# Performance work log

Hardware: AMD Instinct MI355X
Metric: run time of the kernel (lower is better)

Reference implementation:

```python
import jax, jax.numpy as jnp
import numpy as np

B, S, D = 2, 2048, 1024
E, H = 8, 2816  # hidden = 256*ceil(int(2*(4*1024)/3)/256) = 2816
TOP_K = 2


def setup_inputs() -> dict:
    key = jax.random.key(0)
    k0, k1, k2, k3, k4 = jax.random.split(key, 5)
    x = jax.random.normal(k0, (B, S, D), dtype=jnp.float32)
    wg = jax.random.normal(k1, (D, E), dtype=jnp.float32) * (D ** -0.5)
    w1 = jax.random.normal(k2, (E, D, H), dtype=jnp.float32) * 0.02  # gate proj
    w3 = jax.random.normal(k3, (E, D, H), dtype=jnp.float32) * 0.02  # up proj
    w2 = jax.random.normal(k4, (E, H, D), dtype=jnp.float32) * 0.02  # down proj
    return {"x": x, "wg": wg, "w1": w1, "w2": w2, "w3": w3}


def reference(x, wg, w1, w2, w3):
    Bb, Ss, Dd = x.shape
    Ee = w1.shape[0]
    xf = x.reshape(-1, Dd)                       # [T, D]
    logits = xf @ wg                              # [T, E]
    probs = jax.nn.softmax(logits, axis=-1)
    topk_p, topk_i = jax.lax.top_k(probs, TOP_K)  # [T, K]
    topk_p = topk_p / jnp.sum(topk_p, axis=-1, keepdims=True)
    # combine weight per (token, expert): sum over top-k slots
    cw = jnp.sum(jax.nn.one_hot(topk_i, Ee, dtype=xf.dtype) * topk_p[..., None], axis=1)  # [T, E]
    out = jnp.zeros_like(xf)
    for e in range(Ee):  # fixed small loop over experts
        h = jax.nn.silu(xf @ w1[e]) * (xf @ w3[e])   # [T, H] SwiGLU
        out = out + cw[:, e:e + 1] * (h @ w2[e])     # weighted combine
    return out.reshape(Bb, Ss, Dd)
```

## Files before the change

### kernel.cpp

```cpp
#include <hip/hip_runtime.h>
#include <hip/hip_bf16.h>

typedef unsigned short u16;
typedef __bf16 bf16_t;
typedef bf16_t bf16x8 __attribute__((ext_vector_type(8)));
typedef float f32x4 __attribute__((ext_vector_type(4)));

#define T_TOK 4096
#define DIM   1024
#define NEXP  8
#define HID   2816
#define CAP   16

static __device__ __forceinline__ u16 f2b(float f) {
    __hip_bfloat16 h = __float2bfloat16(f);
    return *(u16*)&h;
}

static __device__ __forceinline__ void glds16(const u16* g, u16* l) {
    __builtin_amdgcn_global_load_lds((const __attribute__((address_space(1))) void*)g,
                                     (__attribute__((address_space(3))) void*)l, 16, 0, 0);
}

__global__ void k_gating(const float* __restrict__ X,
                         const float* __restrict__ WG,
                         int* __restrict__ cnt,
                         int* __restrict__ tok,
                         float* __restrict__ wt,
                         u16* __restrict__ Xbf)
{
    int wv   = threadIdx.x >> 6;
    int lane = threadIdx.x & 63;
    int t = blockIdx.x * 4 + wv;
    float l[NEXP];
#pragma unroll
    for (int e = 0; e < NEXP; ++e) l[e] = 0.f;
#pragma unroll
    for (int i = 0; i < DIM/64; ++i) {
        int d = i*64 + lane;
        float xv = X[(size_t)t*DIM + d];
        Xbf[(size_t)t*DIM + d] = f2b(xv);
        const float* wrow = WG + (size_t)d*NEXP;
        float4 wa = *(const float4*)wrow;
        float4 wb = *(const float4*)(wrow + 4);
        l[0] += xv*wa.x; l[1] += xv*wa.y; l[2] += xv*wa.z; l[3] += xv*wa.w;
        l[4] += xv*wb.x; l[5] += xv*wb.y; l[6] += xv*wb.z; l[7] += xv*wb.w;
    }
#pragma unroll
    for (int e = 0; e < NEXP; ++e) {
#pragma unroll
        for (int s = 32; s > 0; s >>= 1)
            l[e] += __shfl_xor(l[e], s, 64);
    }
    if (lane == 0) {
        int i1 = 0; float b1 = l[0];
#pragma unroll
        for (int e = 1; e < NEXP; ++e) if (l[e] > b1) { b1 = l[e]; i1 = e; }
        int i2 = -1; float b2 = 0.f;
#pragma unroll
        for (int e = 0; e < NEXP; ++e) {
            if (e == i1) continue;
            if (i2 < 0 || l[e] > b2) { b2 = l[e]; i2 = e; }
        }
        float p1 = 1.f / (1.f + __expf(b2 - b1));
        float p2 = 1.f - p1;
        int pos = atomicAdd(&cnt[i1], 1);
        tok[i1*T_TOK + pos] = t;  wt[i1*T_TOK + pos] = p1;
        pos = atomicAdd(&cnt[i2], 1);
        tok[i2*T_TOK + pos] = t;  wt[i2*T_TOK + pos] = p2;
    }
}

__global__ void k_compact(const int* __restrict__ cnt,
                          const int* __restrict__ tok, const float* __restrict__ wt,
                          int* __restrict__ ctok, float* __restrict__ cwt)
{
    int e = blockIdx.x;
    int off = 0;
    for (int i = 0; i < e; ++i) off += cnt[i];
    int n = cnt[e];
    for (int i = threadIdx.x; i < n; i += blockDim.x) {
        ctok[off + i] = tok[e*T_TOK + i];
        cwt [off + i] = wt [e*T_TOK + i];
    }
}

#define TS 72
__global__ void k_transpose_cast(const float* __restrict__ in, u16* __restrict__ out,
                                 int R, int C)
{
    __shared__ u16 tle[64*TS];
    size_t mb = (size_t)blockIdx.z * (size_t)R * C;
    int r0 = blockIdx.x * 64, c0 = blockIdx.y * 64;
    int tid = threadIdx.x;
    const float* I = in + mb + (size_t)r0*C + c0;
#pragma unroll
    for (int p = 0; p < 4; ++p) {
        int q = tid + p*256;
        int r = q >> 4, cc = (q & 15) * 4;
        float4 v = *(const float4*)&I[(size_t)r*C + cc];
        tle[(cc+0)*TS + r] = f2b(v.x);
        tle[(cc+1)*TS + r] = f2b(v.y);
        tle[(cc+2)*TS + r] = f2b(v.z);
        tle[(cc+3)*TS + r] = f2b(v.w);
    }
    __syncthreads();
    u16* O = out + mb + (size_t)c0*R + r0;
    int rc = tid & 7, oc = tid >> 3;
#pragma unroll
    for (int p = 0; p < 2; ++p) {
        int c = oc + p*32;
        *(uint4*)&O[(size_t)c*R + rc*8] = *(const uint4*)&tle[c*TS + rc*8];
    }
}

__global__ __launch_bounds__(256, 3) void k_gemm1(
    const u16* __restrict__ X, const u16* __restrict__ W1t, const u16* __restrict__ W3t,
    u16* __restrict__ Hbuf, const int* __restrict__ cnt, const int* __restrict__ ctok)
{
    __shared__ u16 As[128*32];
    __shared__ u16 Bs[128*32];
    __shared__ int tokLds[128];

    const int bid = blockIdx.x;
    const int e   = bid & 7;
    const int q   = bid >> 3;
    const int mt0 = q & (CAP-1);
    const int col = q >> 4;
    const int ne  = cnt[e];
    const int ntile = (ne + 127) >> 7;
    if (mt0 >= ntile) return;
    int off = 0;
    for (int i = 0; i < e; ++i) off += cnt[i];
    const int h0 = col * 64;

    const int tid = threadIdx.x, wave = tid >> 6, lane = tid & 63;
    const int wr = wave >> 1, wc = wave & 1;
    const int quad = lane >> 4, lr = lane & 15;
    const int lrow = lane >> 2, lko = (lane & 3) * 8;

    const size_t wb = (size_t)e * HID * DIM;
    const u16* w1g = W1t + wb + (size_t)(h0 + wave*16 + lrow)*DIM + lko;
    const u16* w3g = W3t + wb + (size_t)(h0 + wave*16 + lrow)*DIM + lko;
    u16* aL0 = &As[(wave*16)*32];
    u16* aL1 = &As[(64 + wave*16)*32];
    u16* bL0 = &Bs[(wave*16)*32];
    u16* bL1 = &Bs[(64 + wave*16)*32];

    for (int tile = mt0; tile < ntile; tile += CAP) {
        const int m0 = tile << 7;
        int nvalid = ne - m0; if (nvalid > 128) nvalid = 128;

        __syncthreads();
        if (tid < 128) {
            int i = (tid < nvalid) ? tid : (nvalid - 1);
            tokLds[tid] = ctok[off + m0 + i];
        }
        __syncthreads();
        const u16* ag0 = X + (size_t)tokLds[wave*16 + lrow]*DIM + lko;
        const u16* ag1 = X + (size_t)tokLds[64 + wave*16 + lrow]*DIM + lko;

        f32x4 a1[4][2], a3[4][2];
#pragma unroll
        for (int m = 0; m < 4; ++m)
#pragma unroll
            for (int n = 0; n < 2; ++n) {
                a1[m][n] = (f32x4){0.f,0.f,0.f,0.f};
                a3[m][n] = (f32x4){0.f,0.f,0.f,0.f};
            }

        for (int k0 = 0; k0 < DIM; k0 += 32) {
            __syncthreads();
            glds16(ag0 + k0, aL0);
            glds16(ag1 + k0, aL1);
            glds16(w1g + k0, bL0);
            glds16(w3g + k0, bL1);
            __syncthreads();
            bf16x8 af[4], b1[2], b3[2];
#pragma unroll
            for (int m = 0; m < 4; ++m)
                af[m] = *(const bf16x8*)&As[(wr*64 + m*16 + lr)*32 + quad*8];
#pragma unroll
            for (int n = 0; n < 2; ++n) {
                b1[n] = *(const bf16x8*)&Bs[(wc*32 + n*16 + lr)*32 + quad*8];
                b3[n] = *(const bf16x8*)&Bs[(64 + wc*32 + n*16 + lr)*32 + quad*8];
            }
#pragma unroll
            for (int m = 0; m < 4; ++m)
#pragma unroll
                for (int n = 0; n < 2; ++n) {
                    a1[m][n] = __builtin_amdgcn_mfma_f32_16x16x32_bf16(af[m], b1[n], a1[m][n], 0, 0, 0);
                    a3[m][n] = __builtin_amdgcn_mfma_f32_16x16x32_bf16(af[m], b3[n], a3[m][n], 0, 0, 0);
                }
        }

#pragma unroll
        for (int m = 0; m < 4; ++m) {
            int mb_ = wr*64 + m*16 + quad*4;
#pragma unroll
            for (int rr = 0; rr < 4; ++rr) {
                int mm = mb_ + rr;
                if (mm >= nvalid) continue;
                u16* hrow = Hbuf + (size_t)(off + m0 + mm)*HID + h0 + wc*32 + lr;
#pragma unroll
                for (int n = 0; n < 2; ++n) {
                    float g = a1[m][n][rr];
                    float u = a3[m][n][rr];
                    hrow[n*16] = f2b((g / (1.f + __expf(-g))) * u);
                }
            }
        }
    }
}

__global__ __launch_bounds__(256, 3) void k_gemm2(
    const u16* __restrict__ Hbuf, const u16* __restrict__ W2t,
    float* __restrict__ outf, const int* __restrict__ cnt,
    const int* __restrict__ ctok, const float* __restrict__ cwt)
{
    __shared__ u16 As[128*32];
    __shared__ u16 Bs[128*32];
    __shared__ int   tLds[128];
    __shared__ float wLds[128];

    const int bid = blockIdx.x;
    const int e   = bid & 7;
    const int q   = bid >> 3;
    const int mt0 = q & (CAP-1);
    const int r2  = q >> 4;
    const int zk  = r2 & 1;
    const int d0  = (r2 >> 1) * 128;
    const int ne  = cnt[e];
    const int ntile = (ne + 127) >> 7;
    if (mt0 >= ntile) return;
    int off = 0;
    for (int i = 0; i < e; ++i) off += cnt[i];
    const int kb = zk * (HID/2);

    const int tid = threadIdx.x, wave = tid >> 6, lane = tid & 63;
    const int wr = wave >> 1, wc = wave & 1;
    const int quad = lane >> 4, lr = lane & 15;
    const int lrow = lane >> 2, lko = (lane & 3) * 8;

    const size_t w2b = (size_t)e * DIM * HID;
    const u16* bg0 = W2t + w2b + (size_t)(d0 + wave*16 + lrow)*HID + kb + lko;
    const u16* bg1 = bg0 + (size_t)64*HID;
    u16* aL0 = &As[(wave*16)*32];
    u16* aL1 = &As[(64 + wave*16)*32];
    u16* bL0 = &Bs[(wave*16)*32];
    u16* bL1 = &Bs[(64 + wave*16)*32];

    for (int tile = mt0; tile < ntile; tile += CAP) {
        const int m0 = tile << 7;
        int nvalid = ne - m0; if (nvalid > 128) nvalid = 128;

        __syncthreads();
        if (tid < 128) {
            int i = (tid < nvalid) ? tid : (nvalid - 1);
            tLds[tid] = ctok[off + m0 + i];
            wLds[tid] = cwt [off + m0 + i];
        }
        __syncthreads();
        int ar0 = wave*16 + lrow;      if (ar0 >= nvalid) ar0 = nvalid - 1;
        int ar1 = 64 + wave*16 + lrow; if (ar1 >= nvalid) ar1 = nvalid - 1;
        const u16* ag0 = Hbuf + (size_t)(off + m0 + ar0)*HID + kb + lko;
        const u16* ag1 = Hbuf + (size_t)(off + m0 + ar1)*HID + kb + lko;

        f32x4 acc[4][4];
#pragma unroll
        for (int a = 0; a < 4; ++a)
#pragma unroll
            for (int b = 0; b < 4; ++b) acc[a][b] = (f32x4){0.f,0.f,0.f,0.f};

        for (int k0 = 0; k0 < HID/2; k0 += 32) {
            __syncthreads();
            glds16(ag0 + k0, aL0);
            glds16(ag1 + k0, aL1);
            glds16(bg0 + k0, bL0);
            glds16(bg1 + k0, bL1);
            __syncthreads();
            bf16x8 af[4], bf[4];
#pragma unroll
            for (int m = 0; m < 4; ++m)
                af[m] = *(const bf16x8*)&As[(wr*64 + m*16 + lr)*32 + quad*8];
#pragma unroll
            for (int n = 0; n < 4; ++n)
                bf[n] = *(const bf16x8*)&Bs[(wc*64 + n*16 + lr)*32 + quad*8];
#pragma unroll
            for (int m = 0; m < 4; ++m)
#pragma unroll
                for (int n = 0; n < 4; ++n)
                    acc[m][n] = __builtin_amdgcn_mfma_f32_16x16x32_bf16(af[m], bf[n], acc[m][n], 0, 0, 0);
        }

#pragma unroll
        for (int m = 0; m < 4; ++m) {
            int mb_ = wr*64 + m*16 + quad*4;
#pragma unroll
            for (int rr = 0; rr < 4; ++rr) {
                int mm = mb_ + rr;
                if (mm >= nvalid) continue;
                float wr_ = wLds[mm];
                float* orow = outf + (size_t)tLds[mm]*DIM + d0 + wc*64 + lr;
#pragma unroll
                for (int n = 0; n < 4; ++n)
                    atomicAdd(&orow[n*16], acc[m][n][rr] * wr_);
            }
        }
    }
}

extern "C" void kernel_launch(void* const* d_in, const int* in_sizes, int n_in,
                              void* d_out, int out_size, void* d_ws, size_t ws_size,
                              hipStream_t stream)
{
    const float* x  = (const float*)d_in[0];
    const float* wg = (const float*)d_in[1];
    const float* w1 = (const float*)d_in[2];
    const float* w2 = (const float*)d_in[3];
    const float* w3 = (const float*)d_in[4];
    float* outf = (float*)d_out;

    char* ws = (char*)d_ws;
    int*   cnt  = (int*)  (ws);
    int*   tok  = (int*)  (ws + 256);
    float* wt   = (float*)(ws + 131328);
    int*   ctok = (int*)  (ws + 262400);
    float* cwt  = (float*)(ws + 295168);
    u16*   Xbf  = (u16*)  (ws + 327936);
    u16*   Hbuf = (u16*)  (ws + 8716544);
    u16*   W1t  = (u16*)  (ws + 54853888);
    u16*   W3t  = (u16*)  (ws + 100991232);
    u16*   W2t  = (u16*)  (ws + 147128576);

    hipMemsetAsync(cnt, 0, 256, stream);
    hipMemsetAsync(outf, 0, (size_t)T_TOK*DIM*sizeof(float), stream);

    k_transpose_cast<<<dim3(DIM/64, HID/64, NEXP), 256, 0, stream>>>(w1, W1t, DIM, HID);
    k_transpose_cast<<<dim3(DIM/64, HID/64, NEXP), 256, 0, stream>>>(w3, W3t, DIM, HID);
    k_transpose_cast<<<dim3(HID/64, DIM/64, NEXP), 256, 0, stream>>>(w2, W2t, HID, DIM);

    k_gating<<<T_TOK/4, 256, 0, stream>>>(x, wg, cnt, tok, wt, Xbf);
    k_compact<<<NEXP, 256, 0, stream>>>(cnt, tok, wt, ctok, cwt);

    k_gemm1<<<NEXP*(HID/64)*CAP, 256, 0, stream>>>(Xbf, W1t, W3t, Hbuf, cnt, ctok);
    k_gemm2<<<NEXP*CAP*2*(DIM/128), 256, 0, stream>>>(Hbuf, W2t, outf, cnt, ctok, cwt);
}
```

Before: 670.0 us.

## Double GEMM K-tile to 64 with XOR-swizzled LDS and fewer M-tile blocks

Both expert GEMM kernels now stage 64-wide K slices in LDS instead of 32, which halves the number of barrier pairs per tile. Each lane now issues four 16-byte direct-to-LDS loads per operand. The 16-byte chunks are XOR-swizzled by row so the MFMA fragment reads avoid LDS bank conflicts. The M-tile cap per expert drops from 16 to 8, so fewer blocks are launched and each loops over more tiles. The trade-off is double the LDS per block, which could limit occupancy, and worse load balance for experts that receive many tokens.

```diff
diff --git a/kernel.cpp b/kernel.cpp
--- a/kernel.cpp
+++ b/kernel.cpp
@@ -10,7 +10,8 @@
 #define DIM   1024
 #define NEXP  8
 #define HID   2816
-#define CAP   16
+#define CAP   8
+#define CAPL  3
 
 static __device__ __forceinline__ u16 f2b(float f) {
     __hip_bfloat16 h = __float2bfloat16(f);
@@ -118,15 +119,15 @@
     const u16* __restrict__ X, const u16* __restrict__ W1t, const u16* __restrict__ W3t,
     u16* __restrict__ Hbuf, const int* __restrict__ cnt, const int* __restrict__ ctok)
 {
-    __shared__ u16 As[128*32];
-    __shared__ u16 Bs[128*32];
+    __shared__ u16 As[128*64];
+    __shared__ u16 Bs[128*64];
     __shared__ int tokLds[128];
 
     const int bid = blockIdx.x;
     const int e   = bid & 7;
     const int q   = bid >> 3;
     const int mt0 = q & (CAP-1);
-    const int col = q >> 4;
+    const int col = q >> CAPL;
     const int ne  = cnt[e];
     const int ntile = (ne + 127) >> 7;
     if (mt0 >= ntile) return;
@@ -137,15 +138,15 @@
     const int tid = threadIdx.x, wave = tid >> 6, lane = tid & 63;
     const int wr = wave >> 1, wc = wave & 1;
     const int quad = lane >> 4, lr = lane & 15;
-    const int lrow = lane >> 2, lko = (lane & 3) * 8;
+    const int lrow8 = lane >> 3;
+    const int sw = ((lane & 7) ^ lrow8) * 8;
 
     const size_t wb = (size_t)e * HID * DIM;
-    const u16* w1g = W1t + wb + (size_t)(h0 + wave*16 + lrow)*DIM + lko;
-    const u16* w3g = W3t + wb + (size_t)(h0 + wave*16 + lrow)*DIM + lko;
-    u16* aL0 = &As[(wave*16)*32];
-    u16* aL1 = &As[(64 + wave*16)*32];
-    u16* bL0 = &Bs[(wave*16)*32];
-    u16* bL1 = &Bs[(64 + wave*16)*32];
+    const u16* Wsel = (wave < 2) ? W1t : W3t;
+    const u16* bp[4];
+#pragma unroll
+    for (int c = 0; c < 4; ++c)
+        bp[c] = Wsel + wb + (size_t)(h0 + (wave & 1)*32 + c*8 + lrow8)*DIM + sw;
 
     for (int tile = mt0; tile < ntile; tile += CAP) {
         const int m0 = tile << 7;
@@ -157,8 +158,10 @@
             tokLds[tid] = ctok[off + m0 + i];
         }
         __syncthreads();
-        const u16* ag0 = X + (size_t)tokLds[wave*16 + lrow]*DIM + lko;
-        const u16* ag1 = X + (size_t)tokLds[64 + wave*16 + lrow]*DIM + lko;
+        const u16* ap[4];
+#pragma unroll
+        for (int c = 0; c < 4; ++c)
+            ap[c] = X + (size_t)tokLds[wave*32 + c*8 + lrow8]*DIM + sw;
 
         f32x4 a1[4][2], a3[4][2];
 #pragma unroll
@@ -169,29 +172,34 @@
                 a3[m][n] = (f32x4){0.f,0.f,0.f,0.f};
             }
 
-        for (int k0 = 0; k0 < DIM; k0 += 32) {
+        for (int k0 = 0; k0 < DIM; k0 += 64) {
             __syncthreads();
-            glds16(ag0 + k0, aL0);
-            glds16(ag1 + k0, aL1);
-            glds16(w1g + k0, bL0);
-            glds16(w3g + k0, bL1);
+#pragma unroll
+            for (int c = 0; c < 4; ++c) {
+                glds16(ap[c] + k0, &As[(wave*32 + c*8)*64]);
+                glds16(bp[c] + k0, &Bs[(wave*32 + c*8)*64]);
+            }
             __syncthreads();
-            bf16x8 af[4], b1[2], b3[2];
-#pragma unroll
-            for (int m = 0; m < 4; ++m)
-                af[m] = *(const bf16x8*)&As[(wr*64 + m*16 + lr)*32 + quad*8];
-#pragma unroll
-            for (int n = 0; n < 2; ++n) {
-                b1[n] = *(const bf16x8*)&Bs[(wc*32 + n*16 + lr)*32 + quad*8];
-                b3[n] = *(const bf16x8*)&Bs[(64 + wc*32 + n*16 + lr)*32 + quad*8];
-            }
-#pragma unroll
-            for (int m = 0; m < 4; ++m)
+#pragma unroll
+            for (int kk = 0; kk < 2; ++kk) {
+                const int jx = ((kk*4 + quad) ^ (lr & 7)) * 8;
+                bf16x8 af[4], b1[2], b3[2];
+#pragma unroll
+                for (int m = 0; m < 4; ++m)
+                    af[m] = *(const bf16x8*)&As[(wr*64 + m*16 + lr)*64 + jx];
 #pragma unroll
                 for (int n = 0; n < 2; ++n) {
-                    a1[m][n] = __builtin_amdgcn_mfma_f32_16x16x32_bf16(af[m], b1[n], a1[m][n], 0, 0, 0);
-                    a3[m][n] = __builtin_amdgcn_mfma_f32_16x16x32_bf16(af[m], b3[n], a3[m][n], 0, 0, 0);
+                    b1[n] = *(const bf16x8*)&Bs[(wc*32 + n*16 + lr)*64 + jx];
+                    b3[n] = *(const bf16x8*)&Bs[(64 + wc*32 + n*16 + lr)*64 + jx];
                 }
+#pragma unroll
+                for (int m = 0; m < 4; ++m)
+#pragma unroll
+                    for (int n = 0; n < 2; ++n) {
+                        a1[m][n] = __builtin_amdgcn_mfma_f32_16x16x32_bf16(af[m], b1[n], a1[m][n], 0, 0, 0);
+                        a3[m][n] = __builtin_amdgcn_mfma_f32_16x16x32_bf16(af[m], b3[n], a3[m][n], 0, 0, 0);
+                    }
+            }
         }
 
 #pragma unroll
@@ -218,8 +226,8 @@
     float* __restrict__ outf, const int* __restrict__ cnt,
     const int* __restrict__ ctok, const float* __restrict__ cwt)
 {
-    __shared__ u16 As[128*32];
-    __shared__ u16 Bs[128*32];
+    __shared__ u16 As[128*64];
+    __shared__ u16 Bs[128*64];
     __shared__ int   tLds[128];
     __shared__ float wLds[128];
 
@@ -227,7 +235,7 @@
     const int e   = bid & 7;
     const int q   = bid >> 3;
     const int mt0 = q & (CAP-1);
-    const int r2  = q >> 4;
+    const int r2  = q >> CAPL;
     const int zk  = r2 & 1;
     const int d0  = (r2 >> 1) * 128;
     const int ne  = cnt[e];
@@ -240,15 +248,14 @@
     const int tid = threadIdx.x, wave = tid >> 6, lane = tid & 63;
     const int wr = wave >> 1, wc = wave & 1;
     const int quad = lane >> 4, lr = lane & 15;
-    const int lrow = lane >> 2, lko = (lane & 3) * 8;
+    const int lrow8 = lane >> 3;
+    const int sw = ((lane & 7) ^ lrow8) * 8;
 
     const size_t w2b = (size_t)e * DIM * HID;
-    const u16* bg0 = W2t + w2b + (size_t)(d0 + wave*16 + lrow)*HID + kb + lko;
-    const u16* bg1 = bg0 + (size_t)64*HID;
-    u16* aL0 = &As[(wave*16)*32];
-    u16* aL1 = &As[(64 + wave*16)*32];
-    u16* bL0 = &Bs[(wave*16)*32];
-    u16* bL1 = &Bs[(64 + wave*16)*32];
+    const u16* bp[4];
+#pragma unroll
+    for (int c = 0; c < 4; ++c)
+        bp[c] = W2t + w2b + (size_t)(d0 + wave*32 + c*8 + lrow8)*HID + kb + sw;
 
     for (int tile = mt0; tile < ntile; tile += CAP) {
         const int m0 = tile << 7;
@@ -261,10 +268,13 @@
             wLds[tid] = cwt [off + m0 + i];
         }
         __syncthreads();
-        int ar0 = wave*16 + lrow;      if (ar0 >= nvalid) ar0 = nvalid - 1;
-        int ar1 = 64 + wave*16 + lrow; if (ar1 >= nvalid) ar1 = nvalid - 1;
-        const u16* ag0 = Hbuf + (size_t)(off + m0 + ar0)*HID + kb + lko;
-        const u16* ag1 = Hbuf + (size_t)(off + m0 + ar1)*HID + kb + lko;
+        const u16* ap[4];
+#pragma unroll
+        for (int c = 0; c < 4; ++c) {
+            int r = wave*32 + c*8 + lrow8;
+            if (r >= nvalid) r = nvalid - 1;
+            ap[c] = Hbuf + (size_t)(off + m0 + r)*HID + kb + sw;
+        }
 
         f32x4 acc[4][4];
 #pragma unroll
@@ -272,25 +282,30 @@
 #pragma unroll
             for (int b = 0; b < 4; ++b) acc[a][b] = (f32x4){0.f,0.f,0.f,0.f};
 
-        for (int k0 = 0; k0 < HID/2; k0 += 32) {
+        for (int k0 = 0; k0 < HID/2; k0 += 64) {
             __syncthreads();
-            glds16(ag0 + k0, aL0);
-            glds16(ag1 + k0, aL1);
-            glds16(bg0 + k0, bL0);
-            glds16(bg1 + k0, bL1);
+#pragma unroll
+            for (int c = 0; c < 4; ++c) {
+                glds16(ap[c] + k0, &As[(wave*32 + c*8)*64]);
+                glds16(bp[c] + k0, &Bs[(wave*32 + c*8)*64]);
+            }
             __syncthreads();
-            bf16x8 af[4], bf[4];
-#pragma unroll
-            for (int m = 0; m < 4; ++m)
-                af[m] = *(const bf16x8*)&As[(wr*64 + m*16 + lr)*32 + quad*8];
-#pragma unroll
-            for (int n = 0; n < 4; ++n)
-                bf[n] = *(const bf16x8*)&Bs[(wc*64 + n*16 + lr)*32 + quad*8];
-#pragma unroll
-            for (int m = 0; m < 4; ++m)
+#pragma unroll
+            for (int kk = 0; kk < 2; ++kk) {
+                const int jx = ((kk*4 + quad) ^ (lr & 7)) * 8;
+                bf16x8 af[4], bf[4];
+#pragma unroll
+                for (int m = 0; m < 4; ++m)
+                    af[m] = *(const bf16x8*)&As[(wr*64 + m*16 + lr)*64 + jx];
 #pragma unroll
                 for (int n = 0; n < 4; ++n)
-                    acc[m][n] = __builtin_amdgcn_mfma_f32_16x16x32_bf16(af[m], bf[n], acc[m][n], 0, 0, 0);
+                    bf[n] = *(const bf16x8*)&Bs[(wc*64 + n*16 + lr)*64 + jx];
+#pragma unroll
+                for (int m = 0; m < 4; ++m)
+#pragma unroll
+                    for (int n = 0; n < 4; ++n)
+                        acc[m][n] = __builtin_amdgcn_mfma_f32_16x16x32_bf16(af[m], bf[n], acc[m][n], 0, 0, 0);
+            }
         }
 
 #pragma unroll
```

Measured after the change: 734.5 us. +9.6%, slower.
